# Performance work log

Hardware: AMD Instinct MI355X
Metric: run time of the kernel (lower is better)

Reference implementation:

```python
import jax, jax.numpy as jnp
import numpy as np

B, T, F = 8192, 336, 8
H = 20        # lstm_hidden_size
DENSE = 20
OUT = 1
N_LAYERS = 3


def _param(key, shape, scale):
    return jax.random.uniform(key, shape, jnp.float32, -scale, scale)


def setup_inputs() -> dict:
    key = jax.random.key(0)
    ks = jax.random.split(key, 32)
    s = 1.0 / np.sqrt(H)
    inp = {"x": jax.random.normal(ks[0], (B, T, F), jnp.float32)}
    k = 1
    for l in range(N_LAYERS):
        in_size = F if l == 0 else H
        inp[f"W_ih{l}"] = _param(ks[k], (4 * H, in_size), s); k += 1
        inp[f"W_hh{l}"] = _param(ks[k], (4 * H, H), s); k += 1
        inp[f"b_ih{l}"] = _param(ks[k], (4 * H,), s); k += 1
        inp[f"b_hh{l}"] = _param(ks[k], (4 * H,), s); k += 1
    inp["fc1_w"] = _param(ks[k], (DENSE, H), 1.0 / np.sqrt(H)); k += 1
    inp["fc1_b"] = _param(ks[k], (DENSE,), 1.0 / np.sqrt(H)); k += 1
    inp["fc2_w"] = _param(ks[k], (OUT, DENSE), 1.0 / np.sqrt(DENSE)); k += 1
    inp["fc2_b"] = _param(ks[k], (OUT,), 1.0 / np.sqrt(DENSE)); k += 1
    return inp


def lstm_layer(x, W_ih, W_hh, b_ih, b_hh):
    """PyTorch-convention LSTM over [B, T, in]; returns hidden sequence [B, T, H]."""
    b = x.shape[0]
    # Precompute input contribution for all timesteps in one GEMM: [B, T, 4H]
    xg = jnp.einsum('bti,gi->btg', x, W_ih) + b_ih + b_hh
    W_hh_T = W_hh.T  # [H, 4H]

    def step(carry, xt):
        h, c = carry
        gates = xt + h @ W_hh_T                      # [B, 4H], gate order i,f,g,o
        i, f, g, o = jnp.split(gates, 4, axis=-1)
        i = jax.nn.sigmoid(i)
        f = jax.nn.sigmoid(f)
        g = jnp.tanh(g)
        o = jax.nn.sigmoid(o)
        c = f * c + i * g
        h = o * jnp.tanh(c)
        return (h, c), h

    h0 = jnp.zeros((b, W_hh.shape[1]), x.dtype)
    c0 = jnp.zeros_like(h0)
    _, hs = jax.lax.scan(step, (h0, c0), jnp.swapaxes(xg, 0, 1))  # [T, B, H]
    return jnp.swapaxes(hs, 0, 1)


def reference(x, W_ih0, W_hh0, b_ih0, b_hh0, W_ih1, W_hh1, b_ih1, b_hh1,
              W_ih2, W_hh2, b_ih2, b_hh2, fc1_w, fc1_b, fc2_w, fc2_b):
    layers = [(W_ih0, W_hh0, b_ih0, b_hh0),
              (W_ih1, W_hh1, b_ih1, b_hh1),
              (W_ih2, W_hh2, b_ih2, b_hh2)]
    h = x
    for (wi, wh, bi, bh) in layers:
        h = lstm_layer(h, wi, wh, bi, bh)
    h = h[:, -1, :]                         # last timestep, [B, H]
    # dropout layers are identity at inference
    h = jax.nn.relu(h @ fc1_w.T + fc1_b)    # [B, DENSE]
    return h @ fc2_w.T + fc2_b              # [B, OUT]
```

## Files before the change

### kernel.cpp

```cpp
#include <hip/hip_runtime.h>


#define T_LEN 336
#define NJ 43

typedef _Float16 f16;
typedef _Float16 f16x4 __attribute__((ext_vector_type(4)));
typedef _Float16 f16x8 __attribute__((ext_vector_type(8)));
typedef float f32x4 __attribute__((ext_vector_type(4)));
typedef int i32x2 __attribute__((ext_vector_type(2)));
typedef int i32x4 __attribute__((ext_vector_type(4)));

#define MFMA(a, b, c) __builtin_amdgcn_mfma_f32_16x16x32_f16((a), (b), (c), 0, 0, 0)

#define SWZ1(n, c) ((c) ^ (((n) & 7) << 3))

#define KS1 1.4426950408889634f
#define KS2 2.8853900817779268f

__device__ __forceinline__ float sigm_p(float y) {
  return __builtin_amdgcn_rcpf(1.0f + __builtin_amdgcn_exp2f(y));
}
__device__ __forceinline__ float tanh_p(float y) {
  return 2.0f * __builtin_amdgcn_rcpf(1.0f + __builtin_amdgcn_exp2f(y)) - 1.0f;
}
__device__ __forceinline__ float tanh_fast(float x) {
  return 2.0f * __builtin_amdgcn_rcpf(1.0f + __builtin_amdgcn_exp2f(-KS2 * x)) - 1.0f;
}

#define CELLS5(DI, DF, DG, DO, DL, HV, HL) {                                                \
  { float i_=sigm_p((DI)[0]), f_=sigm_p((DF)[0]), g_=tanh_p((DG)[0]), o_=sigm_p((DO)[0]);   \
    c0 = f_*c0 + i_*g_; (HV)[0] = (f16)(o_*tanh_fast(c0)); }                                \
  { float i_=sigm_p((DI)[1]), f_=sigm_p((DF)[1]), g_=tanh_p((DG)[1]), o_=sigm_p((DO)[1]);   \
    c1 = f_*c1 + i_*g_; (HV)[1] = (f16)(o_*tanh_fast(c1)); }                                \
  { float i_=sigm_p((DI)[2]), f_=sigm_p((DF)[2]), g_=tanh_p((DG)[2]), o_=sigm_p((DO)[2]);   \
    c2 = f_*c2 + i_*g_; (HV)[2] = (f16)(o_*tanh_fast(c2)); }                                \
  { float i_=sigm_p((DI)[3]), f_=sigm_p((DF)[3]), g_=tanh_p((DG)[3]), o_=sigm_p((DO)[3]);   \
    c3 = f_*c3 + i_*g_; (HV)[3] = (f16)(o_*tanh_fast(c3)); }                                \
  { float i_=sigm_p((DL)[0]), f_=sigm_p((DL)[1]), g_=tanh_p((DL)[2]), o_=sigm_p((DL)[3]);   \
    cL = f_*cL + i_*g_; (HL) = (f16)(o_*tanh_fast(cL)); } }

#define MSTEP_REG(BA, PUB, PC) {                                                            \
  i32x2 _lo = __builtin_bit_cast(i32x2, hvS);                                               \
  int _hlu = (int)(unsigned)__builtin_bit_cast(unsigned short, hlS);                        \
  int _b0 = __builtin_amdgcn_ds_bpermute(adrA, _lo.x);                                      \
  int _b1 = __builtin_amdgcn_ds_bpermute(adrA, _lo.y);                                      \
  int _b2 = __builtin_amdgcn_ds_bpermute(adrB, _lo.x);                                      \
  int _b3 = __builtin_amdgcn_ds_bpermute(adrB, _lo.y);                                      \
  int _hA = __builtin_amdgcn_ds_bpermute(adr0, _hlu);                                       \
  int _hB = __builtin_amdgcn_ds_bpermute(adr1, _hlu);                                       \
  int _hC = __builtin_amdgcn_ds_bpermute(adr2, _hlu);                                       \
  int _hD = __builtin_amdgcn_ds_bpermute(adr3, _hlu);                                       \
  int _w0 = (q < 2) ? _b0 : ((_hA & 0xffff) | (_hB << 16));                                 \
  int _w1 = (q < 2) ? _b1 : ((_hC & 0xffff) | (_hD << 16));                                 \
  i32x4 _bbi = { _w0, _w1, _b2, _b3 };                                                      \
  f16x8 bb = __builtin_bit_cast(f16x8, _bbi);                                               \
  f32x4 di = MFMA(Fb0, bb, MFMA(Fa0, (BA), Bi));                                            \
  f32x4 df = MFMA(Fb1, bb, MFMA(Fa1, (BA), Bf));                                            \
  f32x4 dg = MFMA(Fb2, bb, MFMA(Fa2, (BA), Bg));                                            \
  f32x4 dn = MFMA(Fb3, bb, MFMA(Fa3, (BA), Bo));                                            \
  f32x4 dl = MFMA(Fb4, bb, MFMA(Fa4, (BA), BL));                                            \
  f16x4 hv; f16 hl; CELLS5(di, df, dg, dn, dl, hv, hl)                                      \
  hvS = hv; hlS = hl;                                                                       \
  f16* dp_ = (PUB);                                                                         \
  if (dp_) { *(f16x4*)&dp_[n * 64 + SWZ1(n, (PC) + q * 4)] = hv;                            \
             dp_[n * 64 + SWZ1(n, (PC) + 16 + q)] = hl; } }

#define L0S(SR, SC, DR, DC, PUBP, PC) {                                                     \
  f16x8 b0 = *(const f16x8*)&zT0[SR][n * 64 + SWZ1(n, (SC) + q * 8)];                       \
  f32x4 di = MFMA(Fa0, b0, Bi), df = MFMA(Fa1, b0, Bf), dg = MFMA(Fa2, b0, Bg),             \
        dn = MFMA(Fa3, b0, Bo), dl = MFMA(Fa4, b0, BL);                                     \
  f16x4 hv; f16 hl; CELLS5(di, df, dg, dn, dl, hv, hl)                                      \
  *(f16x4*)&zT0[DR][n * 64 + SWZ1(n, (DC) + 8 + q * 4)] = hv;                               \
  zT0[DR][n * 64 + SWZ1(n, (DC) + 24 + q)] = hl;                                            \
  f16* dp_ = (PUBP);                                                                        \
  *(f16x4*)&dp_[n * 64 + SWZ1(n, (PC) + q * 4)] = hv;                                       \
  dp_[n * 64 + SWZ1(n, (PC) + 16 + q)] = hl; }

__global__ __launch_bounds__(192, 2) void lstm3_ws_kernel(
    const float* __restrict__ x,
    const float* __restrict__ Wih0, const float* __restrict__ Whh0,
    const float* __restrict__ bih0, const float* __restrict__ bhh0,
    const float* __restrict__ Wih1, const float* __restrict__ Whh1,
    const float* __restrict__ bih1, const float* __restrict__ bhh1,
    const float* __restrict__ Wih2, const float* __restrict__ Whh2,
    const float* __restrict__ bih2, const float* __restrict__ bhh2,
    const float* __restrict__ fc1w, const float* __restrict__ fc1b,
    const float* __restrict__ fc2w, const float* __restrict__ fc2b,
    float* __restrict__ out)
{
  __shared__ __align__(16) f16 zT0[4][1024];
  __shared__ __align__(16) f16 zT1[2][4][1024];
  __shared__ __align__(16) f16 zT2[2][4][1024];
  __shared__ __align__(16) float pbuf[64];

  const int tid  = threadIdx.x;
  const int w    = tid >> 6;
  const int lane = tid & 63;
  const int n = lane & 15;
  const int q = lane >> 4;

  const int adrA = 4 * (n + 32 * (q & 1));
  const int adrB = 4 * (n + 16 + 32 * (q & 1));
  const int adr0 = 4 * n, adr1 = 4 * (n + 16), adr2 = 4 * (n + 32), adr3 = 4 * (n + 48);

  {
    f16x8 zer;
#pragma unroll
    for (int j = 0; j < 8; ++j) zer[j] = (f16)0.f;
    for (int i = tid; i < 512; i += 192)  ((f16x8*)&zT0[0][0])[i] = zer;
    for (int i = tid; i < 1024; i += 192) ((f16x8*)&zT1[0][0][0])[i] = zer;
    for (int i = tid; i < 1024; i += 192) ((f16x8*)&zT2[0][0][0])[i] = zer;
  }
  __syncthreads();

  auto rowmap = [](int T, int m) { return T < 4 ? T * 20 + m : (m & 3) * 20 + 16 + (m >> 2); };
  auto gscale = [](int T, int m) {
    int g = (T < 4) ? T : (m & 3);
    return (g == 2) ? -KS2 : -KS1;
  };

  f16x8 Fa0{}, Fa1{}, Fa2{}, Fa3{}, Fa4{};
  f16x8 Fb0{}, Fb1{}, Fb2{}, Fb3{}, Fb4{};
  f32x4 Bi{}, Bf{}, Bg{}, Bo{}, BL{};
  float c0 = 0.f, c1 = 0.f, c2 = 0.f, c3 = 0.f, cL = 0.f;
  f16x4 hvS{};
  f16 hlS = (f16)0.f;

  if (w == 0) {
    auto gA0 = [&](int T) {
      int row = rowmap(T, n);
      float sc = gscale(T, n);
      f16x8 r;
#pragma unroll
      for (int j = 0; j < 8; ++j) {
        int k = q * 8 + j;
        float v = (k < 8) ? Wih0[row * 8 + k] : (k < 28 ? Whh0[row * 20 + k - 8] : 0.f);
        r[j] = (f16)(sc * v);
      }
      return r;
    };
    Fa0 = gA0(0); Fa1 = gA0(1); Fa2 = gA0(2); Fa3 = gA0(3); Fa4 = gA0(4);
    auto gB = [&](int T) {
      f32x4 r;
#pragma unroll
      for (int j = 0; j < 4; ++j) {
        int m = q * 4 + j;
        int row = rowmap(T, m);
        r[j] = gscale(T, m) * (bih0[row] + bhh0[row]);
      }
      return r;
    };
    Bi = gB(0); Bf = gB(1); Bg = gB(2); Bo = gB(3); BL = gB(4);
  } else {
    const float* Wi = (w == 1) ? Wih1 : Wih2;
    const float* Wh = (w == 1) ? Whh1 : Whh2;
    const float* bi = (w == 1) ? bih1 : bih2;
    const float* bh = (w == 1) ? bhh1 : bhh2;
    auto gA = [&](int T, int c) {
      int row = rowmap(T, n);
      float sc = gscale(T, n);
      const float* W = c ? Wh : Wi;
      f16x8 r;
#pragma unroll
      for (int j = 0; j < 8; ++j) {
        int k = q * 8 + j;
        r[j] = (f16)((k < 20) ? sc * W[row * 20 + k] : 0.f);
      }
      return r;
    };
    Fa0 = gA(0, 0); Fb0 = gA(0, 1);
    Fa1 = gA(1, 0); Fb1 = gA(1, 1);
    Fa2 = gA(2, 0); Fb2 = gA(2, 1);
    Fa3 = gA(3, 0); Fb3 = gA(3, 1);
    Fa4 = gA(4, 0); Fb4 = gA(4, 1);
    auto gB = [&](int T) {
      f32x4 r;
#pragma unroll
      for (int j = 0; j < 4; ++j) {
        int m = q * 4 + j;
        int row = rowmap(T, m);
        r[j] = gscale(T, m) * (bi[row] + bh[row]);
      }
      return r;
    };
    Bi = gB(0); Bf = gB(1); Bg = gB(2); Bo = gB(3); BL = gB(4);
  }

  const float* xb = x + (size_t)(blockIdx.x * 16 + n) * (T_LEN * 8) + 4 * q;
  f32x4 xA{}, xB{}, xC{}, xD{};
  if (w == 0) {
    xA = *(const f32x4*)(xb);
    xB = *(const f32x4*)(xb + 16);
    xC = *(const f32x4*)(xb + 32);
    xD = *(const f32x4*)(xb + 48);
  }

#pragma unroll 1
  for (int j = 0; j <= NJ; ++j) {
    asm volatile("" ::: "memory");
    __builtin_amdgcn_s_setprio(1);
    const int wp = j & 1, rp = wp ^ 1;
    if (w == 0) {
      if (j <= 41) {
        f16x4 xh;
        xh[0] = (f16)xA[0]; xh[1] = (f16)xA[1]; xh[2] = (f16)xA[2]; xh[3] = (f16)xA[3];
        *(f16x4*)&zT0[0][n * 64 + SWZ1(n, (q >> 1) * 32 + 4 * (q & 1))] = xh;
        xh[0] = (f16)xB[0]; xh[1] = (f16)xB[1]; xh[2] = (f16)xB[2]; xh[3] = (f16)xB[3];
        *(f16x4*)&zT0[1][n * 64 + SWZ1(n, (q >> 1) * 32 + 4 * (q & 1))] = xh;
        xh[0] = (f16)xC[0]; xh[1] = (f16)xC[1]; xh[2] = (f16)xC[2]; xh[3] = (f16)xC[3];
        *(f16x4*)&zT0[2][n * 64 + SWZ1(n, (q >> 1) * 32 + 4 * (q & 1))] = xh;
        xh[0] = (f16)xD[0]; xh[1] = (f16)xD[1]; xh[2] = (f16)xD[2]; xh[3] = (f16)xD[3];
        *(f16x4*)&zT0[3][n * 64 + SWZ1(n, (q >> 1) * 32 + 4 * (q & 1))] = xh;
        int g = (j + 1 > 41) ? 41 : j + 1;
        xA = *(const f32x4*)(xb + (size_t)(4 * g) * 16);
        xB = *(const f32x4*)(xb + (size_t)(4 * g + 1) * 16);
        xC = *(const f32x4*)(xb + (size_t)(4 * g + 2) * 16);
        xD = *(const f32x4*)(xb + (size_t)(4 * g + 3) * 16);
        f16* p1 = &zT1[wp][0][0];
        L0S(0, 0,  0, 32, p1 + 0 * 1024, 0)
        L0S(0, 32, 1, 0,  p1 + 0 * 1024, 32)
        L0S(1, 0,  1, 32, p1 + 1 * 1024, 0)
        L0S(1, 32, 2, 0,  p1 + 1 * 1024, 32)
        L0S(2, 0,  2, 32, p1 + 2 * 1024, 0)
        L0S(2, 32, 3, 0,  p1 + 2 * 1024, 32)
        L0S(3, 0,  3, 32, p1 + 3 * 1024, 0)
        L0S(3, 32, 0, 0,  p1 + 3 * 1024, 32)
      }
    } else if (w == 1) {
      if (j >= 1 && j <= 42) {
        f16* s1 = &zT1[rp][0][0];
        f16x8 a0 = *(const f16x8*)&s1[0 * 1024 + n * 64 + SWZ1(n, 0  + q * 8)];
        f16x8 a1 = *(const f16x8*)&s1[0 * 1024 + n * 64 + SWZ1(n, 32 + q * 8)];
        f16x8 a2 = *(const f16x8*)&s1[1 * 1024 + n * 64 + SWZ1(n, 0  + q * 8)];
        f16x8 a3 = *(const f16x8*)&s1[1 * 1024 + n * 64 + SWZ1(n, 32 + q * 8)];
        f16x8 a4 = *(const f16x8*)&s1[2 * 1024 + n * 64 + SWZ1(n, 0  + q * 8)];
        f16x8 a5 = *(const f16x8*)&s1[2 * 1024 + n * 64 + SWZ1(n, 32 + q * 8)];
        f16x8 a6 = *(const f16x8*)&s1[3 * 1024 + n * 64 + SWZ1(n, 0  + q * 8)];
        f16x8 a7 = *(const f16x8*)&s1[3 * 1024 + n * 64 + SWZ1(n, 32 + q * 8)];
        f16* p2 = &zT2[wp][0][0];
        MSTEP_REG(a0, p2 + 0 * 1024, 0)
        MSTEP_REG(a1, p2 + 0 * 1024, 32)
        MSTEP_REG(a2, p2 + 1 * 1024, 0)
        MSTEP_REG(a3, p2 + 1 * 1024, 32)
        MSTEP_REG(a4, p2 + 2 * 1024, 0)
        MSTEP_REG(a5, p2 + 2 * 1024, 32)
        MSTEP_REG(a6, p2 + 3 * 1024, 0)
        MSTEP_REG(a7, p2 + 3 * 1024, 32)
      }
    } else {
      if (j >= 2) {
        f16* s2 = &zT2[rp][0][0];
        f16x8 a0 = *(const f16x8*)&s2[0 * 1024 + n * 64 + SWZ1(n, 0  + q * 8)];
        f16x8 a1 = *(const f16x8*)&s2[0 * 1024 + n * 64 + SWZ1(n, 32 + q * 8)];
        f16x8 a2 = *(const f16x8*)&s2[1 * 1024 + n * 64 + SWZ1(n, 0  + q * 8)];
        f16x8 a3 = *(const f16x8*)&s2[1 * 1024 + n * 64 + SWZ1(n, 32 + q * 8)];
        f16x8 a4 = *(const f16x8*)&s2[2 * 1024 + n * 64 + SWZ1(n, 0  + q * 8)];
        f16x8 a5 = *(const f16x8*)&s2[2 * 1024 + n * 64 + SWZ1(n, 32 + q * 8)];
        f16x8 a6 = *(const f16x8*)&s2[3 * 1024 + n * 64 + SWZ1(n, 0  + q * 8)];
        f16x8 a7 = *(const f16x8*)&s2[3 * 1024 + n * 64 + SWZ1(n, 32 + q * 8)];
        MSTEP_REG(a0, (f16*)nullptr, 0)
        MSTEP_REG(a1, (f16*)nullptr, 0)
        MSTEP_REG(a2, (f16*)nullptr, 0)
        MSTEP_REG(a3, (f16*)nullptr, 0)
        MSTEP_REG(a4, (f16*)nullptr, 0)
        MSTEP_REG(a5, (f16*)nullptr, 0)
        MSTEP_REG(a6, (f16*)nullptr, 0)
        MSTEP_REG(a7, (f16*)nullptr, 0)
      }
    }
    __builtin_amdgcn_s_setprio(0);
    asm volatile("s_waitcnt lgkmcnt(0)\n\ts_barrier" ::: "memory");
  }

  if (w == 2) {
    *(f16x4*)&zT2[1][0][n * 64 + SWZ1(n, 32 + q * 4)] = hvS;
    zT2[1][0][n * 64 + SWZ1(n, 48 + q)] = hlS;
    asm volatile("s_waitcnt lgkmcnt(0)" ::: "memory");
    const f16* hb = &zT2[1][0][0];
    f16x4 hv0 = *(const f16x4*)&hb[n * 64 + SWZ1(n, 32)];
    f16x4 hv1 = *(const f16x4*)&hb[n * 64 + SWZ1(n, 36)];
    f16x4 hv2 = *(const f16x4*)&hb[n * 64 + SWZ1(n, 40)];
    f16x4 hv3 = *(const f16x4*)&hb[n * 64 + SWZ1(n, 44)];
    f16x4 hv4 = *(const f16x4*)&hb[n * 64 + SWZ1(n, 48)];
    float p = 0.f;
#pragma unroll
    for (int i = 0; i < 5; ++i) {
      int d = q * 5 + i;
      const float* wr = fc1w + d * 20;
      float s = fc1b[d]
        + wr[0]  * (float)hv0[0] + wr[1]  * (float)hv0[1] + wr[2]  * (float)hv0[2] + wr[3]  * (float)hv0[3]
        + wr[4]  * (float)hv1[0] + wr[5]  * (float)hv1[1] + wr[6]  * (float)hv1[2] + wr[7]  * (float)hv1[3]
        + wr[8]  * (float)hv2[0] + wr[9]  * (float)hv2[1] + wr[10] * (float)hv2[2] + wr[11] * (float)hv2[3]
        + wr[12] * (float)hv3[0] + wr[13] * (float)hv3[1] + wr[14] * (float)hv3[2] + wr[15] * (float)hv3[3]
        + wr[16] * (float)hv4[0] + wr[17] * (float)hv4[1] + wr[18] * (float)hv4[2] + wr[19] * (float)hv4[3];
      p += fc2w[d] * fmaxf(s, 0.f);
    }
    pbuf[n * 4 + q] = p;
    if (q == 0) {
      f32x4 pv = *(const f32x4*)&pbuf[n * 4];
      out[blockIdx.x * 16 + n] = pv[0] + pv[1] + pv[2] + pv[3] + fc2b[0];
    }
  }
}

extern "C" void kernel_launch(void* const* d_in, const int* in_sizes, int n_in,
                              void* d_out, int out_size, void* d_ws, size_t ws_size,
                              hipStream_t stream) {
  const float* x    = (const float*)d_in[0];
  const float* Wih0 = (const float*)d_in[1];
  const float* Whh0 = (const float*)d_in[2];
  const float* bih0 = (const float*)d_in[3];
  const float* bhh0 = (const float*)d_in[4];
  const float* Wih1 = (const float*)d_in[5];
  const float* Whh1 = (const float*)d_in[6];
  const float* bih1 = (const float*)d_in[7];
  const float* bhh1 = (const float*)d_in[8];
  const float* Wih2 = (const float*)d_in[9];
  const float* Whh2 = (const float*)d_in[10];
  const float* bih2 = (const float*)d_in[11];
  const float* bhh2 = (const float*)d_in[12];
  const float* fc1w = (const float*)d_in[13];
  const float* fc1b = (const float*)d_in[14];
  const float* fc2w = (const float*)d_in[15];
  const float* fc2b = (const float*)d_in[16];
  float* out = (float*)d_out;

  hipLaunchKernelGGL(lstm3_ws_kernel, dim3(8192 / 16), dim3(192), 0, stream,
                     x, Wih0, Whh0, bih0, bhh0,
                     Wih1, Whh1, bih1, bhh1,
                     Wih2, Whh2, bih2, bhh2,
                     fc1w, fc1b, fc2w, fc2b, out);
}
```

Baseline: 386.2 us.

## Feed recurrent hidden state to MFMA directly from registers, dropping LDS round-trips

The recurrent h@W_hh contribution now comes from 16x16x16 MFMAs. These take the per-lane hidden-state registers as the B operand, using W_hh fragments rearranged to match the lane layout, so the ds_bpermute shuffles in layers 1 and 2 are no longer needed. Layer 0 likewise stops staging x and h through the zT0 LDS ring; it converts x to f16 in registers and splits W_ih into even/odd fragments. The aim is to take LDS and permute latency off the serial recurrence critical path. The cost is more and smaller MFMAs per step, plus extra weight registers.

After: 380.4 us. Within noise of the previous version (-1.5%).

```diff
diff --git a/kernel.cpp b/kernel.cpp
--- a/kernel.cpp
+++ b/kernel.cpp
@@ -8,10 +8,9 @@
 typedef _Float16 f16x4 __attribute__((ext_vector_type(4)));
 typedef _Float16 f16x8 __attribute__((ext_vector_type(8)));
 typedef float f32x4 __attribute__((ext_vector_type(4)));
-typedef int i32x2 __attribute__((ext_vector_type(2)));
-typedef int i32x4 __attribute__((ext_vector_type(4)));
 
 #define MFMA(a, b, c) __builtin_amdgcn_mfma_f32_16x16x32_f16((a), (b), (c), 0, 0, 0)
+#define M16(a, b, c)  __builtin_amdgcn_mfma_f32_16x16x16f16((a), (b), (c), 0, 0, 0)
 
 #define SWZ1(n, c) ((c) ^ (((n) & 7) << 3))
 
@@ -40,42 +39,39 @@
   { float i_=sigm_p((DL)[0]), f_=sigm_p((DL)[1]), g_=tanh_p((DL)[2]), o_=sigm_p((DL)[3]);   \
     cL = f_*cL + i_*g_; (HL) = (f16)(o_*tanh_fast(cL)); } }
 
-#define MSTEP_REG(BA, PUB, PC) {                                                            \
-  i32x2 _lo = __builtin_bit_cast(i32x2, hvS);                                               \
-  int _hlu = (int)(unsigned)__builtin_bit_cast(unsigned short, hlS);                        \
-  int _b0 = __builtin_amdgcn_ds_bpermute(adrA, _lo.x);                                      \
-  int _b1 = __builtin_amdgcn_ds_bpermute(adrA, _lo.y);                                      \
-  int _b2 = __builtin_amdgcn_ds_bpermute(adrB, _lo.x);                                      \
-  int _b3 = __builtin_amdgcn_ds_bpermute(adrB, _lo.y);                                      \
-  int _hA = __builtin_amdgcn_ds_bpermute(adr0, _hlu);                                       \
-  int _hB = __builtin_amdgcn_ds_bpermute(adr1, _hlu);                                       \
-  int _hC = __builtin_amdgcn_ds_bpermute(adr2, _hlu);                                       \
-  int _hD = __builtin_amdgcn_ds_bpermute(adr3, _hlu);                                       \
-  int _w0 = (q < 2) ? _b0 : ((_hA & 0xffff) | (_hB << 16));                                 \
-  int _w1 = (q < 2) ? _b1 : ((_hC & 0xffff) | (_hD << 16));                                 \
-  i32x4 _bbi = { _w0, _w1, _b2, _b3 };                                                      \
-  f16x8 bb = __builtin_bit_cast(f16x8, _bbi);                                               \
-  f32x4 di = MFMA(Fb0, bb, MFMA(Fa0, (BA), Bi));                                            \
-  f32x4 df = MFMA(Fb1, bb, MFMA(Fa1, (BA), Bf));                                            \
-  f32x4 dg = MFMA(Fb2, bb, MFMA(Fa2, (BA), Bg));                                            \
-  f32x4 dn = MFMA(Fb3, bb, MFMA(Fa3, (BA), Bo));                                            \
-  f32x4 dl = MFMA(Fb4, bb, MFMA(Fa4, (BA), BL));                                            \
+#define HFOLD(T0, T1, T2, T3, T4, DI, DF, DG, DN, DL) {                                     \
+  f16x4 bm = hvS;                                                                           \
+  f16x4 bl; bl[0] = hlS; bl[1] = hlS; bl[2] = hlS; bl[3] = hlS;                             \
+  DI = M16(Hl0, bl, M16(Hm0, bm, T0));                                                      \
+  DF = M16(Hl1, bl, M16(Hm1, bm, T1));                                                      \
+  DG = M16(Hl2, bl, M16(Hm2, bm, T2));                                                      \
+  DN = M16(Hl3, bl, M16(Hm3, bm, T3));                                                      \
+  DL = M16(Hl4, bl, M16(Hm4, bm, T4)); }
+
+#define PUBLISH(PUBP, PC, HV, HL) {                                                         \
+  f16* dp_ = (PUBP);                                                                        \
+  if (dp_) { *(f16x4*)&dp_[n * 64 + SWZ1(n, (PC) + q * 4)] = (HV);                          \
+             dp_[n * 64 + SWZ1(n, (PC) + 16 + q)] = (HL); } }
+
+#define L0R(XP, XF, PUBP, PC) {                                                             \
+  f32x4 t0 = M16(XP##0, (XF), Bi), t1 = M16(XP##1, (XF), Bf),                               \
+        t2 = M16(XP##2, (XF), Bg), t3 = M16(XP##3, (XF), Bo),                               \
+        t4 = M16(XP##4, (XF), BL);                                                          \
+  f32x4 di, df, dg, dn, dl;                                                                 \
+  HFOLD(t0, t1, t2, t3, t4, di, df, dg, dn, dl)                                             \
   f16x4 hv; f16 hl; CELLS5(di, df, dg, dn, dl, hv, hl)                                      \
   hvS = hv; hlS = hl;                                                                       \
-  f16* dp_ = (PUB);                                                                         \
-  if (dp_) { *(f16x4*)&dp_[n * 64 + SWZ1(n, (PC) + q * 4)] = hv;                            \
-             dp_[n * 64 + SWZ1(n, (PC) + 16 + q)] = hl; } }
-
-#define L0S(SR, SC, DR, DC, PUBP, PC) {                                                     \
-  f16x8 b0 = *(const f16x8*)&zT0[SR][n * 64 + SWZ1(n, (SC) + q * 8)];                       \
-  f32x4 di = MFMA(Fa0, b0, Bi), df = MFMA(Fa1, b0, Bf), dg = MFMA(Fa2, b0, Bg),             \
-        dn = MFMA(Fa3, b0, Bo), dl = MFMA(Fa4, b0, BL);                                     \
+  PUBLISH(PUBP, PC, hv, hl) }
+
+#define MSTEP_R(BA, PUBP, PC) {                                                             \
+  f32x4 t0 = MFMA(Fa0, (BA), Bi), t1 = MFMA(Fa1, (BA), Bf),                                 \
+        t2 = MFMA(Fa2, (BA), Bg), t3 = MFMA(Fa3, (BA), Bo),                                 \
+        t4 = MFMA(Fa4, (BA), BL);                                                           \
+  f32x4 di, df, dg, dn, dl;                                                                 \
+  HFOLD(t0, t1, t2, t3, t4, di, df, dg, dn, dl)                                             \
   f16x4 hv; f16 hl; CELLS5(di, df, dg, dn, dl, hv, hl)                                      \
-  *(f16x4*)&zT0[DR][n * 64 + SWZ1(n, (DC) + 8 + q * 4)] = hv;                               \
-  zT0[DR][n * 64 + SWZ1(n, (DC) + 24 + q)] = hl;                                            \
-  f16* dp_ = (PUBP);                                                                        \
-  *(f16x4*)&dp_[n * 64 + SWZ1(n, (PC) + q * 4)] = hv;                                       \
-  dp_[n * 64 + SWZ1(n, (PC) + 16 + q)] = hl; }
+  hvS = hv; hlS = hl;                                                                       \
+  PUBLISH(PUBP, PC, hv, hl) }
 
 __global__ __launch_bounds__(192, 2) void lstm3_ws_kernel(
     const float* __restrict__ x,
@@ -89,7 +85,6 @@
     const float* __restrict__ fc2w, const float* __restrict__ fc2b,
     float* __restrict__ out)
 {
-  __shared__ __align__(16) f16 zT0[4][1024];
   __shared__ __align__(16) f16 zT1[2][4][1024];
   __shared__ __align__(16) f16 zT2[2][4][1024];
   __shared__ __align__(16) float pbuf[64];
@@ -100,15 +95,10 @@
   const int n = lane & 15;
   const int q = lane >> 4;
 
-  const int adrA = 4 * (n + 32 * (q & 1));
-  const int adrB = 4 * (n + 16 + 32 * (q & 1));
-  const int adr0 = 4 * n, adr1 = 4 * (n + 16), adr2 = 4 * (n + 32), adr3 = 4 * (n + 48);
-
   {
     f16x8 zer;
 #pragma unroll
     for (int j = 0; j < 8; ++j) zer[j] = (f16)0.f;
-    for (int i = tid; i < 512; i += 192)  ((f16x8*)&zT0[0][0])[i] = zer;
     for (int i = tid; i < 1024; i += 192) ((f16x8*)&zT1[0][0][0])[i] = zer;
     for (int i = tid; i < 1024; i += 192) ((f16x8*)&zT2[0][0][0])[i] = zer;
   }
@@ -120,71 +110,91 @@
     return (g == 2) ? -KS2 : -KS1;
   };
 
+  const float* WiP = (w == 0) ? Wih0 : (w == 1) ? Wih1 : Wih2;
+  const float* WhP = (w == 0) ? Whh0 : (w == 1) ? Whh1 : Whh2;
+  const float* biP = (w == 0) ? bih0 : (w == 1) ? bih1 : bih2;
+  const float* bhP = (w == 0) ? bhh0 : (w == 1) ? bhh1 : bhh2;
+
   f16x8 Fa0{}, Fa1{}, Fa2{}, Fa3{}, Fa4{};
-  f16x8 Fb0{}, Fb1{}, Fb2{}, Fb3{}, Fb4{};
+  f16x4 Xe0{}, Xe1{}, Xe2{}, Xe3{}, Xe4{};
+  f16x4 Xo0{}, Xo1{}, Xo2{}, Xo3{}, Xo4{};
+  f16x4 Hm0{}, Hm1{}, Hm2{}, Hm3{}, Hm4{};
+  f16x4 Hl0{}, Hl1{}, Hl2{}, Hl3{}, Hl4{};
   f32x4 Bi{}, Bf{}, Bg{}, Bo{}, BL{};
   float c0 = 0.f, c1 = 0.f, c2 = 0.f, c3 = 0.f, cL = 0.f;
   f16x4 hvS{};
   f16 hlS = (f16)0.f;
 
-  if (w == 0) {
-    auto gA0 = [&](int T) {
-      int row = rowmap(T, n);
-      float sc = gscale(T, n);
-      f16x8 r;
-#pragma unroll
-      for (int j = 0; j < 8; ++j) {
-        int k = q * 8 + j;
-        float v = (k < 8) ? Wih0[row * 8 + k] : (k < 28 ? Whh0[row * 20 + k - 8] : 0.f);
-        r[j] = (f16)(sc * v);
-      }
-      return r;
-    };
-    Fa0 = gA0(0); Fa1 = gA0(1); Fa2 = gA0(2); Fa3 = gA0(3); Fa4 = gA0(4);
+  {
+    auto gM = [&](int T) {
+      int row = rowmap(T, n);
+      float sc = gscale(T, n);
+      f16x4 r;
+#pragma unroll
+      for (int j = 0; j < 4; ++j) r[j] = (f16)(sc * WhP[row * 20 + q * 4 + j]);
+      return r;
+    };
+    auto gL = [&](int T) {
+      int row = rowmap(T, n);
+      float sc = gscale(T, n);
+      f16x4 r;
+      r[0] = (f16)(sc * WhP[row * 20 + 16 + q]);
+      r[1] = (f16)0.f; r[2] = (f16)0.f; r[3] = (f16)0.f;
+      return r;
+    };
+    Hm0 = gM(0); Hm1 = gM(1); Hm2 = gM(2); Hm3 = gM(3); Hm4 = gM(4);
+    Hl0 = gL(0); Hl1 = gL(1); Hl2 = gL(2); Hl3 = gL(3); Hl4 = gL(4);
     auto gB = [&](int T) {
       f32x4 r;
 #pragma unroll
       for (int j = 0; j < 4; ++j) {
         int m = q * 4 + j;
         int row = rowmap(T, m);
-        r[j] = gscale(T, m) * (bih0[row] + bhh0[row]);
+        r[j] = gscale(T, m) * (biP[row] + bhP[row]);
       }
       return r;
     };
     Bi = gB(0); Bf = gB(1); Bg = gB(2); Bo = gB(3); BL = gB(4);
+  }
+
+  if (w == 0) {
+    auto gXE = [&](int T) {
+      int row = rowmap(T, n);
+      float sc = gscale(T, n);
+      f16x4 r;
+#pragma unroll
+      for (int j = 0; j < 4; ++j) {
+        int k = q * 4 + j;
+        r[j] = (f16)((k < 8) ? sc * WiP[row * 8 + k] : 0.f);
+      }
+      return r;
+    };
+    auto gXO = [&](int T) {
+      int row = rowmap(T, n);
+      float sc = gscale(T, n);
+      f16x4 r;
+#pragma unroll
+      for (int j = 0; j < 4; ++j) {
+        int k = q * 4 + j;
+        r[j] = (f16)((k >= 8) ? sc * WiP[row * 8 + k - 8] : 0.f);
+      }
+      return r;
+    };
+    Xe0 = gXE(0); Xe1 = gXE(1); Xe2 = gXE(2); Xe3 = gXE(3); Xe4 = gXE(4);
+    Xo0 = gXO(0); Xo1 = gXO(1); Xo2 = gXO(2); Xo3 = gXO(3); Xo4 = gXO(4);
   } else {
-    const float* Wi = (w == 1) ? Wih1 : Wih2;
-    const float* Wh = (w == 1) ? Whh1 : Whh2;
-    const float* bi = (w == 1) ? bih1 : bih2;
-    const float* bh = (w == 1) ? bhh1 : bhh2;
-    auto gA = [&](int T, int c) {
-      int row = rowmap(T, n);
-      float sc = gscale(T, n);
-      const float* W = c ? Wh : Wi;
+    auto gA = [&](int T) {
+      int row = rowmap(T, n);
+      float sc = gscale(T, n);
       f16x8 r;
 #pragma unroll
       for (int j = 0; j < 8; ++j) {
         int k = q * 8 + j;
-        r[j] = (f16)((k < 20) ? sc * W[row * 20 + k] : 0.f);
-      }
-      return r;
-    };
-    Fa0 = gA(0, 0); Fb0 = gA(0, 1);
-    Fa1 = gA(1, 0); Fb1 = gA(1, 1);
-    Fa2 = gA(2, 0); Fb2 = gA(2, 1);
-    Fa3 = gA(3, 0); Fb3 = gA(3, 1);
-    Fa4 = gA(4, 0); Fb4 = gA(4, 1);
-    auto gB = [&](int T) {
-      f32x4 r;
-#pragma unroll
-      for (int j = 0; j < 4; ++j) {
-        int m = q * 4 + j;
-        int row = rowmap(T, m);
-        r[j] = gscale(T, m) * (bi[row] + bh[row]);
-      }
-      return r;
-    };
-    Bi = gB(0); Bf = gB(1); Bg = gB(2); Bo = gB(3); BL = gB(4);
+        r[j] = (f16)((k < 20) ? sc * WiP[row * 20 + k] : 0.f);
+      }
+      return r;
+    };
+    Fa0 = gA(0); Fa1 = gA(1); Fa2 = gA(2); Fa3 = gA(3); Fa4 = gA(4);
   }
 
   const float* xb = x + (size_t)(blockIdx.x * 16 + n) * (T_LEN * 8) + 4 * q;
@@ -203,29 +213,25 @@
     const int wp = j & 1, rp = wp ^ 1;
     if (w == 0) {
       if (j <= 41) {
-        f16x4 xh;
-        xh[0] = (f16)xA[0]; xh[1] = (f16)xA[1]; xh[2] = (f16)xA[2]; xh[3] = (f16)xA[3];
-        *(f16x4*)&zT0[0][n * 64 + SWZ1(n, (q >> 1) * 32 + 4 * (q & 1))] = xh;
-        xh[0] = (f16)xB[0]; xh[1] = (f16)xB[1]; xh[2] = (f16)xB[2]; xh[3] = (f16)xB[3];
-        *(f16x4*)&zT0[1][n * 64 + SWZ1(n, (q >> 1) * 32 + 4 * (q & 1))] = xh;
-        xh[0] = (f16)xC[0]; xh[1] = (f16)xC[1]; xh[2] = (f16)xC[2]; xh[3] = (f16)xC[3];
-        *(f16x4*)&zT0[2][n * 64 + SWZ1(n, (q >> 1) * 32 + 4 * (q & 1))] = xh;
-        xh[0] = (f16)xD[0]; xh[1] = (f16)xD[1]; xh[2] = (f16)xD[2]; xh[3] = (f16)xD[3];
-        *(f16x4*)&zT0[3][n * 64 + SWZ1(n, (q >> 1) * 32 + 4 * (q & 1))] = xh;
+        f16x4 xf0, xf1, xf2, xf3;
+        xf0[0] = (f16)xA[0]; xf0[1] = (f16)xA[1]; xf0[2] = (f16)xA[2]; xf0[3] = (f16)xA[3];
+        xf1[0] = (f16)xB[0]; xf1[1] = (f16)xB[1]; xf1[2] = (f16)xB[2]; xf1[3] = (f16)xB[3];
+        xf2[0] = (f16)xC[0]; xf2[1] = (f16)xC[1]; xf2[2] = (f16)xC[2]; xf2[3] = (f16)xC[3];
+        xf3[0] = (f16)xD[0]; xf3[1] = (f16)xD[1]; xf3[2] = (f16)xD[2]; xf3[3] = (f16)xD[3];
         int g = (j + 1 > 41) ? 41 : j + 1;
         xA = *(const f32x4*)(xb + (size_t)(4 * g) * 16);
         xB = *(const f32x4*)(xb + (size_t)(4 * g + 1) * 16);
         xC = *(const f32x4*)(xb + (size_t)(4 * g + 2) * 16);
         xD = *(const f32x4*)(xb + (size_t)(4 * g + 3) * 16);
         f16* p1 = &zT1[wp][0][0];
-        L0S(0, 0,  0, 32, p1 + 0 * 1024, 0)
-        L0S(0, 32, 1, 0,  p1 + 0 * 1024, 32)
-        L0S(1, 0,  1, 32, p1 + 1 * 1024, 0)
-        L0S(1, 32, 2, 0,  p1 + 1 * 1024, 32)
-        L0S(2, 0,  2, 32, p1 + 2 * 1024, 0)
-        L0S(2, 32, 3, 0,  p1 + 2 * 1024, 32)
-        L0S(3, 0,  3, 32, p1 + 3 * 1024, 0)
-        L0S(3, 32, 0, 0,  p1 + 3 * 1024, 32)
+        L0R(Xe, xf0, p1 + 0 * 1024, 0)
+        L0R(Xo, xf0, p1 + 0 * 1024, 32)
+        L0R(Xe, xf1, p1 + 1 * 1024, 0)
+        L0R(Xo, xf1, p1 + 1 * 1024, 32)
+        L0R(Xe, xf2, p1 + 2 * 1024, 0)
+        L0R(Xo, xf2, p1 + 2 * 1024, 32)
+        L0R(Xe, xf3, p1 + 3 * 1024, 0)
+        L0R(Xo, xf3, p1 + 3 * 1024, 32)
       }
     } else if (w == 1) {
       if (j >= 1 && j <= 42) {
@@ -239,14 +245,14 @@
         f16x8 a6 = *(const f16x8*)&s1[3 * 1024 + n * 64 + SWZ1(n, 0  + q * 8)];
         f16x8 a7 = *(const f16x8*)&s1[3 * 1024 + n * 64 + SWZ1(n, 32 + q * 8)];
         f16* p2 = &zT2[wp][0][0];
-        MSTEP_REG(a0, p2 + 0 * 1024, 0)
-        MSTEP_REG(a1, p2 + 0 * 1024, 32)
-        MSTEP_REG(a2, p2 + 1 * 1024, 0)
-        MSTEP_REG(a3, p2 + 1 * 1024, 32)
-        MSTEP_REG(a4, p2 + 2 * 1024, 0)
-        MSTEP_REG(a5, p2 + 2 * 1024, 32)
-        MSTEP_REG(a6, p2 + 3 * 1024, 0)
-        MSTEP_REG(a7, p2 + 3 * 1024, 32)
+        MSTEP_R(a0, p2 + 0 * 1024, 0)
+        MSTEP_R(a1, p2 + 0 * 1024, 32)
+        MSTEP_R(a2, p2 + 1 * 1024, 0)
+        MSTEP_R(a3, p2 + 1 * 1024, 32)
+        MSTEP_R(a4, p2 + 2 * 1024, 0)
+        MSTEP_R(a5, p2 + 2 * 1024, 32)
+        MSTEP_R(a6, p2 + 3 * 1024, 0)
+        MSTEP_R(a7, p2 + 3 * 1024, 32)
       }
     } else {
       if (j >= 2) {
@@ -259,14 +265,14 @@
         f16x8 a5 = *(const f16x8*)&s2[2 * 1024 + n * 64 + SWZ1(n, 32 + q * 8)];
         f16x8 a6 = *(const f16x8*)&s2[3 * 1024 + n * 64 + SWZ1(n, 0  + q * 8)];
         f16x8 a7 = *(const f16x8*)&s2[3 * 1024 + n * 64 + SWZ1(n, 32 + q * 8)];
-        MSTEP_REG(a0, (f16*)nullptr, 0)
-        MSTEP_REG(a1, (f16*)nullptr, 0)
-        MSTEP_REG(a2, (f16*)nullptr, 0)
-        MSTEP_REG(a3, (f16*)nullptr, 0)
-        MSTEP_REG(a4, (f16*)nullptr, 0)
-        MSTEP_REG(a5, (f16*)nullptr, 0)
-        MSTEP_REG(a6, (f16*)nullptr, 0)
-        MSTEP_REG(a7, (f16*)nullptr, 0)
+        MSTEP_R(a0, (f16*)nullptr, 0)
+        MSTEP_R(a1, (f16*)nullptr, 0)
+        MSTEP_R(a2, (f16*)nullptr, 0)
+        MSTEP_R(a3, (f16*)nullptr, 0)
+        MSTEP_R(a4, (f16*)nullptr, 0)
+        MSTEP_R(a5, (f16*)nullptr, 0)
+        MSTEP_R(a6, (f16*)nullptr, 0)
+        MSTEP_R(a7, (f16*)nullptr, 0)
       }
     }
     __builtin_amdgcn_s_setprio(0);
```
